# Kernel tuning notes

Measured on AMD Instinct MI355X. Metric: run time of the kernel, lower is better.

Reference implementation:

```python
import jax, jax.numpy as jnp
import numpy as np

GROUPS = 8
NEG_SLOPE = 0.1
EPS = 1e-5


def group_norm(x, gamma, beta):
    # x: (B, N, C). Matches torch GroupNorm applied on (B, C, N):
    # normalize over (channels-in-group, N) per batch per group.
    B, N, C = x.shape
    xg = x.reshape(B, N, GROUPS, C // GROUPS)
    mean = xg.mean(axis=(1, 3), keepdims=True)
    var = xg.var(axis=(1, 3), keepdims=True)
    xg = (xg - mean) * jax.lax.rsqrt(var + EPS)
    return xg.reshape(B, N, C) * gamma + beta


def unary_block(x, W, b, gamma, beta):
    # Linear -> GroupNorm -> LeakyReLU(0.1)
    h = jnp.einsum('bnc,cd->bnd', x, W) + b
    h = group_norm(h, gamma, beta)
    return jnp.where(h >= 0, h, NEG_SLOPE * h)


def setup_inputs() -> dict:
    key = jax.random.key(0)
    ks = jax.random.split(key, 16)
    B, N, M, K, Cin, Cout = 4, 8192, 32768, 16, 128, 128
    inp = {
        'q_feats': jax.random.normal(ks[0], (B, N, Cin), jnp.float32),
        's_feats': jax.random.normal(ks[1], (B, M, Cin), jnp.float32),
        'q_points': jax.random.normal(ks[2], (B, N, 3), jnp.float32),
        's_points': jax.random.normal(ks[3], (B, N, K, 3), jnp.float32),
        'downsample_indices': jax.random.randint(ks[4], (B, N, K), 0, M, jnp.int32),
    }
    sc1 = 1.0 / np.sqrt(Cin)
    sc2 = 1.0 / np.sqrt(Cout)
    inp['W1'] = jax.random.uniform(ks[5], (Cin, Cout), jnp.float32, -sc1, sc1)
    inp['b1'] = jnp.zeros((Cout,), jnp.float32)
    inp['g1'] = jnp.ones((Cout,), jnp.float32)
    inp['be1'] = jnp.zeros((Cout,), jnp.float32)
    inp['W2'] = jax.random.uniform(ks[6], (Cout, Cout), jnp.float32, -sc2, sc2)
    inp['b2'] = jnp.zeros((Cout,), jnp.float32)
    inp['g2'] = jnp.ones((Cout,), jnp.float32)
    inp['be2'] = jnp.zeros((Cout,), jnp.float32)
    inp['W3'] = jax.random.uniform(ks[7], (Cout, Cout), jnp.float32, -sc2, sc2)
    inp['b3'] = jnp.zeros((Cout,), jnp.float32)
    inp['g3'] = jnp.ones((Cout,), jnp.float32)
    inp['be3'] = jnp.zeros((Cout,), jnp.float32)
    return inp


def reference(q_feats, s_feats, q_points, s_points, downsample_indices,
              W1, b1, g1, be1, W2, b2, g2, be2, W3, b3, g3, be3):
    # knn_gather: (B, N, K, C) gathered from (B, M, C)
    grouped = jax.vmap(lambda f, i: f[i])(s_feats, downsample_indices)
    # inverse-squared-distance weights over K neighbors
    d2 = jnp.sum((s_points - q_points[:, :, None, :]) ** 2, axis=-1)  # (B,N,K)
    w = 1.0 / (d2 + 1e-8)
    w = w / jnp.sum(w, axis=-1, keepdims=True)
    latent = jnp.sum(grouped * w[..., None], axis=2)  # (B,N,C)
    h = unary_block(latent, W1, b1, g1, be1)
    h = unary_block(h, W2, b2, g2, be2)
    return unary_block(h + q_feats, W3, b3, g3, be3)
```

## Files before the change

kernel.cpp:

```cpp
#include <hip/hip_runtime.h>


constexpr int NPB = 8192;
constexpr int BN  = 32768;
constexpr int CH  = 128;
constexpr int KNB = 16;
constexpr int MS  = 32768;
constexpr int NG  = 8;
constexpr int CG  = 16;
constexpr int RPB = 64;
constexpr int NBLK = BN / RPB;
constexpr int BPB  = NPB / RPB;
constexpr int XS = 144;
constexpr int WS = 144;

typedef short short8 __attribute__((ext_vector_type(8)));
typedef float floatx4 __attribute__((ext_vector_type(4)));

__device__ __forceinline__ unsigned short f2bs(float f) {
    unsigned int u = __builtin_bit_cast(unsigned int, f);
    unsigned int r = (u + 0x7fffu + ((u >> 16) & 1u)) >> 16;
    return (unsigned short)r;
}
__device__ __forceinline__ float bs2f(unsigned short s) {
    unsigned int u = ((unsigned int)s) << 16;
    return __builtin_bit_cast(float, u);
}

__global__ __launch_bounds__(256) void k_prep(
    const float* __restrict__ W1, const float* __restrict__ W2,
    const float* __restrict__ W3,
    unsigned short* __restrict__ Wt1, unsigned short* __restrict__ Wt2,
    unsigned short* __restrict__ Wt3)
{
    const int bi = blockIdx.x;
    const int w  = bi >> 6;
    const int i  = bi & 63;
    const int el = i * 256 + threadIdx.x;
    const int n  = el >> 7, k = el & 127;
    const float* W = (w == 0) ? W1 : (w == 1) ? W2 : W3;
    unsigned short* Wt = (w == 0) ? Wt1 : (w == 1) ? Wt2 : Wt3;
    Wt[n * 128 + k] = f2bs(W[k * 128 + n]);
}

template <int MODE>
__global__ __launch_bounds__(256) void k_pass(
    const unsigned short* __restrict__ hin,
    const float* __restrict__ part_in,
    const float* __restrict__ gamma,
    const float* __restrict__ beta,
    const float* __restrict__ qf,
    const float* __restrict__ sf,
    const float* __restrict__ qp,
    const float* __restrict__ sp,
    const int*   __restrict__ idx,
    const unsigned short* __restrict__ Wt,
    const float* __restrict__ bias,
    unsigned short* __restrict__ hout,
    float* __restrict__ part_out)
{
    const int bi = blockIdx.x;
    const int t  = threadIdx.x;
    const int b  = bi / BPB;

    __shared__ unsigned short Xl[RPB * XS];
    __shared__ unsigned short Wl[CH * WS];
    __shared__ float red[16][17];
    __shared__ float2 stats_s[NG];
    __shared__ float wv[RPB * KNB];
    __shared__ float winv[RPB];
    __shared__ float pw[4][16];

    #pragma unroll
    for (int i = 0; i < 8; i++) {
        int el = i * 2048 + t * 8;
        short8 w8 = *(const short8*)(Wt + el);
        *(short8*)&Wl[(el >> 7) * WS + (el & 127)] = w8;
    }

    if (MODE == 0) {
        #pragma unroll
        for (int i = 0; i < 4; i++) {
            int p = i * 256 + t;
            int row = p >> 4, k = p & 15;
            size_t rg = (size_t)bi * RPB + row;
            float qx = qp[rg * 3 + 0], qy = qp[rg * 3 + 1], qz = qp[rg * 3 + 2];
            const float* spp = sp + (rg * KNB + k) * 3;
            float dx = spp[0] - qx, dy = spp[1] - qy, dz = spp[2] - qz;
            wv[p] = 1.0f / (dx * dx + dy * dy + dz * dz + 1e-8f);
        }
        __syncthreads();
        if (t < RPB) {
            float s = 0.f;
            #pragma unroll
            for (int k = 0; k < KNB; k++) s += wv[t * KNB + k];
            winv[t] = 1.0f / s;
        }
        __syncthreads();
        const int grp = t >> 5, c4 = (t & 31) * 4;
        for (int rr = 0; rr < 8; rr++) {
            int row = grp * 8 + rr;
            size_t rg = (size_t)bi * RPB + row;
            const int* ip = idx + rg * KNB;
            float ax = 0.f, ay = 0.f, az = 0.f, aw = 0.f;
            #pragma unroll
            for (int k = 0; k < KNB; k++) {
                int j = ip[k];
                const float4 f = *(const float4*)(sf + ((size_t)b * MS + j) * CH + c4);
                float w = wv[row * KNB + k];
                ax += w * f.x; ay += w * f.y; az += w * f.z; aw += w * f.w;
            }
            float wi = winv[row];
            ushort4 pk;
            pk.x = f2bs(ax * wi); pk.y = f2bs(ay * wi);
            pk.z = f2bs(az * wi); pk.w = f2bs(aw * wi);
            *(ushort4*)&Xl[row * XS + c4] = pk;
        }
    } else {
        {
            int j = t & 15, chunk = t >> 4;
            float acc = 0.f;
            #pragma unroll
            for (int i = 0; i < 8; i++)
                acc += part_in[(size_t)(b * BPB + chunk * 8 + i) * 16 + j];
            red[chunk][j] = acc;
        }
        __syncthreads();
        if (t < NG) {
            float s = 0.f, q = 0.f;
            #pragma unroll
            for (int c = 0; c < 16; c++) { s += red[c][t]; q += red[c][t + 8]; }
            const float cnt = (float)(NPB * CG);
            float mean = s / cnt;
            float var  = q / cnt - mean * mean;
            stats_s[t] = make_float2(mean, rsqrtf(var + 1e-5f));
        }
        __syncthreads();
        #pragma unroll
        for (int i = 0; i < 4; i++) {
            int flat = i * 2048 + t * 8;
            int row = flat >> 7, col = flat & 127;
            size_t gidx = (size_t)bi * RPB * CH + flat;
            short8 hv = *(const short8*)(hin + gidx);
            float2 st = stats_s[col >> 4];
            float4 g0 = *(const float4*)(gamma + col);
            float4 g1 = *(const float4*)(gamma + col + 4);
            float4 b0 = *(const float4*)(beta + col);
            float4 b1 = *(const float4*)(beta + col + 4);
            float gg[8] = {g0.x, g0.y, g0.z, g0.w, g1.x, g1.y, g1.z, g1.w};
            float bb[8] = {b0.x, b0.y, b0.z, b0.w, b1.x, b1.y, b1.z, b1.w};
            float re[8];
            if (MODE == 2) {
                float4 r0 = *(const float4*)(qf + gidx);
                float4 r1 = *(const float4*)(qf + gidx + 4);
                re[0]=r0.x; re[1]=r0.y; re[2]=r0.z; re[3]=r0.w;
                re[4]=r1.x; re[5]=r1.y; re[6]=r1.z; re[7]=r1.w;
            }
            unsigned short ov[8];
            #pragma unroll
            for (int e = 0; e < 8; e++) {
                float v = bs2f((unsigned short)hv[e]);
                float y = (v - st.x) * st.y * gg[e] + bb[e];
                y = (y >= 0.f) ? y : 0.1f * y;
                if (MODE == 2) y += re[e];
                ov[e] = f2bs(y);
            }
            *(short8*)&Xl[row * XS + col] = *(short8*)ov;
        }
    }
    __syncthreads();

    const int w  = t >> 6;
    const int l  = t & 63;
    const int lr = l & 15;
    const int qd = l >> 4;
    floatx4 acc[8] = {};
    #pragma unroll
    for (int kt = 0; kt < 4; kt++) {
        short8 a = *(const short8*)&Xl[(w * 16 + lr) * XS + kt * 32 + qd * 8];
        #pragma unroll
        for (int j = 0; j < 8; j++) {
            short8 bf = *(const short8*)&Wl[(j * 16 + lr) * WS + kt * 32 + qd * 8];
            acc[j] = __builtin_amdgcn_mfma_f32_16x16x32_bf16(a, bf, acc[j], 0, 0, 0);
        }
    }

    float vals[8][4];
    #pragma unroll
    for (int j = 0; j < 8; j++) {
        float bj = bias[j * 16 + lr];
        float ss = 0.f, qq = 0.f;
        #pragma unroll
        for (int r = 0; r < 4; r++) {
            float v = acc[j][r] + bj;
            vals[j][r] = v;
            ss += v; qq += v * v;
        }
        #pragma unroll
        for (int off = 32; off; off >>= 1) {
            ss += __shfl_down(ss, off);
            qq += __shfl_down(qq, off);
        }
        if (l == 0) { pw[w][j] = ss; pw[w][8 + j] = qq; }
    }
    #pragma unroll
    for (int j = 0; j < 8; j++)
        #pragma unroll
        for (int r = 0; r < 4; r++)
            Xl[(w * 16 + qd * 4 + r) * XS + j * 16 + lr] = f2bs(vals[j][r]);
    __syncthreads();
    if (t < 16)
        part_out[(size_t)bi * 16 + t] = pw[0][t] + pw[1][t] + pw[2][t] + pw[3][t];
    #pragma unroll
    for (int i = 0; i < 4; i++) {
        int flat = i * 2048 + t * 8;
        int row = flat >> 7, col = flat & 127;
        *(short8*)(hout + (size_t)bi * RPB * CH + flat) =
            *(const short8*)&Xl[row * XS + col];
    }
}

__global__ __launch_bounds__(256) void k_out(
    const unsigned short* __restrict__ hin, const float* __restrict__ part_in,
    const float* __restrict__ gamma, const float* __restrict__ beta,
    float* __restrict__ out)
{
    const int bi = blockIdx.x;
    const int t  = threadIdx.x;
    const int b  = bi / BPB;
    __shared__ float red[16][17];
    __shared__ float2 stats_s[NG];
    {
        int j = t & 15, chunk = t >> 4;
        float acc = 0.f;
        #pragma unroll
        for (int i = 0; i < 8; i++)
            acc += part_in[(size_t)(b * BPB + chunk * 8 + i) * 16 + j];
        red[chunk][j] = acc;
    }
    __syncthreads();
    if (t < NG) {
        float s = 0.f, q = 0.f;
        #pragma unroll
        for (int c = 0; c < 16; c++) { s += red[c][t]; q += red[c][t + 8]; }
        const float cnt = (float)(NPB * CG);
        float mean = s / cnt;
        float var  = q / cnt - mean * mean;
        stats_s[t] = make_float2(mean, rsqrtf(var + 1e-5f));
    }
    __syncthreads();
    #pragma unroll
    for (int i = 0; i < 4; i++) {
        int flat = i * 2048 + t * 8;
        int col = flat & 127;
        size_t gidx = (size_t)bi * RPB * CH + flat;
        short8 hv = *(const short8*)(hin + gidx);
        float2 st = stats_s[col >> 4];
        float4 g0 = *(const float4*)(gamma + col);
        float4 g1 = *(const float4*)(gamma + col + 4);
        float4 b0 = *(const float4*)(beta + col);
        float4 b1 = *(const float4*)(beta + col + 4);
        float gg[8] = {g0.x, g0.y, g0.z, g0.w, g1.x, g1.y, g1.z, g1.w};
        float bb[8] = {b0.x, b0.y, b0.z, b0.w, b1.x, b1.y, b1.z, b1.w};
        float o[8];
        #pragma unroll
        for (int e = 0; e < 8; e++) {
            float v = bs2f((unsigned short)hv[e]);
            float y = (v - st.x) * st.y * gg[e] + bb[e];
            o[e] = (y >= 0.f) ? y : 0.1f * y;
        }
        float4 o0 = {o[0], o[1], o[2], o[3]};
        float4 o1 = {o[4], o[5], o[6], o[7]};
        *(float4*)(out + gidx)     = o0;
        *(float4*)(out + gidx + 4) = o1;
    }
}

extern "C" void kernel_launch(void* const* d_in, const int* in_sizes, int n_in,
                              void* d_out, int out_size, void* d_ws, size_t ws_size,
                              hipStream_t stream) {
    const float* qf  = (const float*)d_in[0];
    const float* sf  = (const float*)d_in[1];
    const float* qp  = (const float*)d_in[2];
    const float* sp  = (const float*)d_in[3];
    const int*   idx = (const int*)  d_in[4];
    const float* W1  = (const float*)d_in[5];
    const float* b1  = (const float*)d_in[6];
    const float* g1  = (const float*)d_in[7];
    const float* be1 = (const float*)d_in[8];
    const float* W2  = (const float*)d_in[9];
    const float* b2  = (const float*)d_in[10];
    const float* g2  = (const float*)d_in[11];
    const float* be2 = (const float*)d_in[12];
    const float* W3  = (const float*)d_in[13];
    const float* b3  = (const float*)d_in[14];
    const float* g3  = (const float*)d_in[15];
    const float* be3 = (const float*)d_in[16];

    char* ws = (char*)d_ws;
    unsigned short* Wt1 = (unsigned short*)(ws);
    unsigned short* Wt2 = (unsigned short*)(ws + 32768);
    unsigned short* Wt3 = (unsigned short*)(ws + 65536);
    float* p1 = (float*)(ws + 98304);
    float* p2 = (float*)(ws + 131072);
    float* p3 = (float*)(ws + 163840);
    unsigned short* h1 = (unsigned short*)(ws + 196608);
    unsigned short* h2 = (unsigned short*)(ws + 196608 + 8388608);
    unsigned short* h3 = (unsigned short*)(ws + 196608 + 2 * 8388608);
    float* out = (float*)d_out;

    k_prep<<<192, 256, 0, stream>>>(W1, W2, W3, Wt1, Wt2, Wt3);
    k_pass<0><<<NBLK, 256, 0, stream>>>(nullptr, nullptr, nullptr, nullptr,
                                        nullptr, sf, qp, sp, idx,
                                        Wt1, b1, h1, p1);
    k_pass<1><<<NBLK, 256, 0, stream>>>(h1, p1, g1, be1, nullptr,
                                        nullptr, nullptr, nullptr, nullptr,
                                        Wt2, b2, h2, p2);
    k_pass<2><<<NBLK, 256, 0, stream>>>(h2, p2, g2, be2, qf,
                                        nullptr, nullptr, nullptr, nullptr,
                                        Wt3, b3, h3, p3);
    k_out<<<NBLK, 256, 0, stream>>>(h3, p3, g3, be3, out);
}
```

Measured before the change: 195.4 us.

## Fuse all three unary blocks into one persistent kernel with grid barriers

Replaces the four per-stage kernels with a single kernel that holds each block's GEMM output in registers across stages. Group-norm statistics are accumulated with global atomics, and an atomic-counter grid barrier separates the stages. This removes the bf16 intermediate writes and reads to global memory and the extra kernel launches, and remaps block indices so each XCD handles one batch. It also pads the LDS row stride. In exchange it depends on all 512 blocks being resident at once to avoid deadlock, and the float atomics make the statistics summation order nondeterministic.

```diff
diff --git a/kernel.cpp b/kernel.cpp
--- a/kernel.cpp
+++ b/kernel.cpp
@@ -11,29 +11,39 @@
 constexpr int RPB = 64;
 constexpr int NBLK = BN / RPB;
 constexpr int BPB  = NPB / RPB;
-constexpr int XS = 144;
-constexpr int WS = 144;
+constexpr int XS = 152;
+constexpr int WS = 152;
 
 typedef short short8 __attribute__((ext_vector_type(8)));
 typedef float floatx4 __attribute__((ext_vector_type(4)));
 
-__device__ __forceinline__ unsigned short f2bs(float f) {
+static __device__ __forceinline__ unsigned short f2bs(float f) {
     unsigned int u = __builtin_bit_cast(unsigned int, f);
     unsigned int r = (u + 0x7fffu + ((u >> 16) & 1u)) >> 16;
     return (unsigned short)r;
 }
-__device__ __forceinline__ float bs2f(unsigned short s) {
-    unsigned int u = ((unsigned int)s) << 16;
-    return __builtin_bit_cast(float, u);
+
+static __device__ __forceinline__ void gbar(unsigned int* bar, unsigned int target) {
+    __syncthreads();
+    if (threadIdx.x == 0) {
+        __hip_atomic_fetch_add(bar, 1u, __ATOMIC_ACQ_REL, __HIP_MEMORY_SCOPE_AGENT);
+        unsigned int v;
+        do {
+            __builtin_amdgcn_s_sleep(2);
+            v = __hip_atomic_load(bar, __ATOMIC_ACQUIRE, __HIP_MEMORY_SCOPE_AGENT);
+        } while (v < target);
+    }
+    __syncthreads();
 }
 
 __global__ __launch_bounds__(256) void k_prep(
     const float* __restrict__ W1, const float* __restrict__ W2,
     const float* __restrict__ W3,
     unsigned short* __restrict__ Wt1, unsigned short* __restrict__ Wt2,
-    unsigned short* __restrict__ Wt3)
+    unsigned short* __restrict__ Wt3, float* __restrict__ accs)
 {
     const int bi = blockIdx.x;
+    if (bi == 0) accs[threadIdx.x] = 0.f;
     const int w  = bi >> 6;
     const int i  = bi & 63;
     const int el = i * 256 + threadIdx.x;
@@ -43,60 +53,129 @@
     Wt[n * 128 + k] = f2bs(W[k * 128 + n]);
 }
 
-template <int MODE>
-__global__ __launch_bounds__(256) void k_pass(
-    const unsigned short* __restrict__ hin,
-    const float* __restrict__ part_in,
-    const float* __restrict__ gamma,
-    const float* __restrict__ beta,
+__global__ __launch_bounds__(256, 2) void k_fused(
+    const float* __restrict__ sf, const float* __restrict__ qp,
+    const float* __restrict__ sp, const int* __restrict__ idx,
     const float* __restrict__ qf,
-    const float* __restrict__ sf,
-    const float* __restrict__ qp,
-    const float* __restrict__ sp,
-    const int*   __restrict__ idx,
-    const unsigned short* __restrict__ Wt,
-    const float* __restrict__ bias,
-    unsigned short* __restrict__ hout,
-    float* __restrict__ part_out)
+    const unsigned short* __restrict__ Wt1,
+    const unsigned short* __restrict__ Wt2,
+    const unsigned short* __restrict__ Wt3,
+    const float* __restrict__ b1, const float* __restrict__ g1, const float* __restrict__ be1,
+    const float* __restrict__ b2, const float* __restrict__ g2, const float* __restrict__ be2,
+    const float* __restrict__ b3, const float* __restrict__ g3, const float* __restrict__ be3,
+    float* __restrict__ accs,
+    unsigned int* __restrict__ bar,
+    float* __restrict__ out)
 {
-    const int bi = blockIdx.x;
-    const int t  = threadIdx.x;
-    const int b  = bi / BPB;
+    const int p   = blockIdx.x;
+    const int xcd = p & 7, q = p >> 3;
+    const int bi  = (xcd >> 1) * BPB + (xcd & 1) * 64 + q;
+    const int b   = xcd >> 1;
+    const int t   = threadIdx.x;
+    const int w   = t >> 6;
+    const int l   = t & 63;
+    const int lr  = l & 15;
+    const int qd  = l >> 4;
 
     __shared__ unsigned short Xl[RPB * XS];
     __shared__ unsigned short Wl[CH * WS];
-    __shared__ float red[16][17];
     __shared__ float2 stats_s[NG];
     __shared__ float wv[RPB * KNB];
     __shared__ float winv[RPB];
     __shared__ float pw[4][16];
 
+    float vals[8][4];
+
+    auto stageW = [&](const unsigned short* __restrict__ Wt) {
+        #pragma unroll
+        for (int i = 0; i < 8; i++) {
+            int el = i * 2048 + t * 8;
+            short8 w8 = *(const short8*)(Wt + el);
+            *(short8*)&Wl[(el >> 7) * WS + (el & 127)] = w8;
+        }
+    };
+
+    auto do_gemm = [&](const float* __restrict__ bias, float* accL) {
+        floatx4 acc[8] = {};
+        #pragma unroll
+        for (int kt = 0; kt < 4; kt++) {
+            short8 a = *(const short8*)&Xl[(w * 16 + lr) * XS + kt * 32 + qd * 8];
+            #pragma unroll
+            for (int j = 0; j < 8; j++) {
+                short8 bf = *(const short8*)&Wl[(j * 16 + lr) * WS + kt * 32 + qd * 8];
+                acc[j] = __builtin_amdgcn_mfma_f32_16x16x32_bf16(a, bf, acc[j], 0, 0, 0);
+            }
+        }
+        #pragma unroll
+        for (int j = 0; j < 8; j++) {
+            float bj = bias[j * 16 + lr];
+            float ss = 0.f, qq = 0.f;
+            #pragma unroll
+            for (int r = 0; r < 4; r++) {
+                float v = acc[j][r] + bj;
+                vals[j][r] = v;
+                ss += v; qq += v * v;
+            }
+            #pragma unroll
+            for (int off = 32; off; off >>= 1) {
+                ss += __shfl_down(ss, off);
+                qq += __shfl_down(qq, off);
+            }
+            if (l == 0) { pw[w][j] = ss; pw[w][8 + j] = qq; }
+        }
+        __syncthreads();
+        if (t < 16)
+            atomicAdd(&accL[b * 16 + t], pw[0][t] + pw[1][t] + pw[2][t] + pw[3][t]);
+    };
+
+    auto gn_apply = [&](float* accL, const float* __restrict__ g,
+                        const float* __restrict__ be, const float* __restrict__ resid) {
+        if (t < 8) {
+            float s  = __hip_atomic_load(accL + b * 16 + t,     __ATOMIC_ACQUIRE, __HIP_MEMORY_SCOPE_AGENT);
+            float q2 = __hip_atomic_load(accL + b * 16 + 8 + t, __ATOMIC_ACQUIRE, __HIP_MEMORY_SCOPE_AGENT);
+            const float cnt = (float)(NPB * CG);
+            float mean = s / cnt;
+            float var  = q2 / cnt - mean * mean;
+            stats_s[t] = make_float2(mean, rsqrtf(var + 1e-5f));
+        }
+        __syncthreads();
+        #pragma unroll
+        for (int j = 0; j < 8; j++) {
+            const int c = j * 16 + lr;
+            float2 st = stats_s[j];
+            float ga = g[c], bb = be[c];
+            #pragma unroll
+            for (int r = 0; r < 4; r++) {
+                float y = (vals[j][r] - st.x) * st.y * ga + bb;
+                y = (y >= 0.f) ? y : 0.1f * y;
+                if (resid)
+                    y += resid[((size_t)bi * RPB + w * 16 + qd * 4 + r) * CH + c];
+                Xl[(w * 16 + qd * 4 + r) * XS + c] = f2bs(y);
+            }
+        }
+        __syncthreads();
+    };
+
+    stageW(Wt1);
     #pragma unroll
-    for (int i = 0; i < 8; i++) {
-        int el = i * 2048 + t * 8;
-        short8 w8 = *(const short8*)(Wt + el);
-        *(short8*)&Wl[(el >> 7) * WS + (el & 127)] = w8;
-    }
-
-    if (MODE == 0) {
-        #pragma unroll
-        for (int i = 0; i < 4; i++) {
-            int p = i * 256 + t;
-            int row = p >> 4, k = p & 15;
-            size_t rg = (size_t)bi * RPB + row;
-            float qx = qp[rg * 3 + 0], qy = qp[rg * 3 + 1], qz = qp[rg * 3 + 2];
-            const float* spp = sp + (rg * KNB + k) * 3;
-            float dx = spp[0] - qx, dy = spp[1] - qy, dz = spp[2] - qz;
-            wv[p] = 1.0f / (dx * dx + dy * dy + dz * dz + 1e-8f);
-        }
-        __syncthreads();
-        if (t < RPB) {
-            float s = 0.f;
-            #pragma unroll
-            for (int k = 0; k < KNB; k++) s += wv[t * KNB + k];
-            winv[t] = 1.0f / s;
-        }
-        __syncthreads();
+    for (int i = 0; i < 4; i++) {
+        int pk = i * 256 + t;
+        int row = pk >> 4, k = pk & 15;
+        size_t rg = (size_t)bi * RPB + row;
+        float qx = qp[rg * 3 + 0], qy = qp[rg * 3 + 1], qz = qp[rg * 3 + 2];
+        const float* spp = sp + (rg * KNB + k) * 3;
+        float dx = spp[0] - qx, dy = spp[1] - qy, dz = spp[2] - qz;
+        wv[pk] = 1.0f / (dx * dx + dy * dy + dz * dz + 1e-8f);
+    }
+    __syncthreads();
+    if (t < RPB) {
+        float s = 0.f;
+        #pragma unroll
+        for (int k = 0; k < KNB; k++) s += wv[t * KNB + k];
+        winv[t] = 1.0f / s;
+    }
+    __syncthreads();
+    {
         const int grp = t >> 5, c4 = (t & 31) * 4;
         for (int rr = 0; rr < 8; rr++) {
             int row = grp * 8 + rr;
@@ -107,172 +186,51 @@
             for (int k = 0; k < KNB; k++) {
                 int j = ip[k];
                 const float4 f = *(const float4*)(sf + ((size_t)b * MS + j) * CH + c4);
-                float w = wv[row * KNB + k];
-                ax += w * f.x; ay += w * f.y; az += w * f.z; aw += w * f.w;
+                float ww = wv[row * KNB + k];
+                ax += ww * f.x; ay += ww * f.y; az += ww * f.z; aw += ww * f.w;
             }
             float wi = winv[row];
-            ushort4 pk;
-            pk.x = f2bs(ax * wi); pk.y = f2bs(ay * wi);
-            pk.z = f2bs(az * wi); pk.w = f2bs(aw * wi);
-            *(ushort4*)&Xl[row * XS + c4] = pk;
-        }
-    } else {
-        {
-            int j = t & 15, chunk = t >> 4;
-            float acc = 0.f;
-            #pragma unroll
-            for (int i = 0; i < 8; i++)
-                acc += part_in[(size_t)(b * BPB + chunk * 8 + i) * 16 + j];
-            red[chunk][j] = acc;
-        }
-        __syncthreads();
-        if (t < NG) {
-            float s = 0.f, q = 0.f;
-            #pragma unroll
-            for (int c = 0; c < 16; c++) { s += red[c][t]; q += red[c][t + 8]; }
-            const float cnt = (float)(NPB * CG);
-            float mean = s / cnt;
-            float var  = q / cnt - mean * mean;
-            stats_s[t] = make_float2(mean, rsqrtf(var + 1e-5f));
-        }
-        __syncthreads();
-        #pragma unroll
-        for (int i = 0; i < 4; i++) {
-            int flat = i * 2048 + t * 8;
-            int row = flat >> 7, col = flat & 127;
-            size_t gidx = (size_t)bi * RPB * CH + flat;
-            short8 hv = *(const short8*)(hin + gidx);
-            float2 st = stats_s[col >> 4];
-            float4 g0 = *(const float4*)(gamma + col);
-            float4 g1 = *(const float4*)(gamma + col + 4);
-            float4 b0 = *(const float4*)(beta + col);
-            float4 b1 = *(const float4*)(beta + col + 4);
-            float gg[8] = {g0.x, g0.y, g0.z, g0.w, g1.x, g1.y, g1.z, g1.w};
-            float bb[8] = {b0.x, b0.y, b0.z, b0.w, b1.x, b1.y, b1.z, b1.w};
-            float re[8];
-            if (MODE == 2) {
-                float4 r0 = *(const float4*)(qf + gidx);
-                float4 r1 = *(const float4*)(qf + gidx + 4);
-                re[0]=r0.x; re[1]=r0.y; re[2]=r0.z; re[3]=r0.w;
-                re[4]=r1.x; re[5]=r1.y; re[6]=r1.z; re[7]=r1.w;
-            }
-            unsigned short ov[8];
-            #pragma unroll
-            for (int e = 0; e < 8; e++) {
-                float v = bs2f((unsigned short)hv[e]);
-                float y = (v - st.x) * st.y * gg[e] + bb[e];
-                y = (y >= 0.f) ? y : 0.1f * y;
-                if (MODE == 2) y += re[e];
-                ov[e] = f2bs(y);
-            }
-            *(short8*)&Xl[row * XS + col] = *(short8*)ov;
-        }
-    }
-    __syncthreads();
-
-    const int w  = t >> 6;
-    const int l  = t & 63;
-    const int lr = l & 15;
-    const int qd = l >> 4;
-    floatx4 acc[8] = {};
-    #pragma unroll
-    for (int kt = 0; kt < 4; kt++) {
-        short8 a = *(const short8*)&Xl[(w * 16 + lr) * XS + kt * 32 + qd * 8];
-        #pragma unroll
-        for (int j = 0; j < 8; j++) {
-            short8 bf = *(const short8*)&Wl[(j * 16 + lr) * WS + kt * 32 + qd * 8];
-            acc[j] = __builtin_amdgcn_mfma_f32_16x16x32_bf16(a, bf, acc[j], 0, 0, 0);
-        }
-    }
-
-    float vals[8][4];
+            ushort4 pkv;
+            pkv.x = f2bs(ax * wi); pkv.y = f2bs(ay * wi);
+            pkv.z = f2bs(az * wi); pkv.w = f2bs(aw * wi);
+            *(ushort4*)&Xl[row * XS + c4] = pkv;
+        }
+    }
+    __syncthreads();
+
+    do_gemm(b1, accs + 0);
+    stageW(Wt2);
+    gbar(bar, 1 * NBLK);
+
+    gn_apply(accs + 0, g1, be1, nullptr);
+    do_gemm(b2, accs + 64);
+    stageW(Wt3);
+    gbar(bar, 2 * NBLK);
+
+    gn_apply(accs + 64, g2, be2, qf);
+    do_gemm(b3, accs + 128);
+    gbar(bar, 3 * NBLK);
+
+    if (t < 8) {
+        float s  = __hip_atomic_load(accs + 128 + b * 16 + t,     __ATOMIC_ACQUIRE, __HIP_MEMORY_SCOPE_AGENT);
+        float q2 = __hip_atomic_load(accs + 128 + b * 16 + 8 + t, __ATOMIC_ACQUIRE, __HIP_MEMORY_SCOPE_AGENT);
+        const float cnt = (float)(NPB * CG);
+        float mean = s / cnt;
+        float var  = q2 / cnt - mean * mean;
+        stats_s[t] = make_float2(mean, rsqrtf(var + 1e-5f));
+    }
+    __syncthreads();
     #pragma unroll
     for (int j = 0; j < 8; j++) {
-        float bj = bias[j * 16 + lr];
-        float ss = 0.f, qq = 0.f;
+        const int c = j * 16 + lr;
+        float2 st = stats_s[j];
+        float ga = g3[c], bb = be3[c];
         #pragma unroll
         for (int r = 0; r < 4; r++) {
-            float v = acc[j][r] + bj;
-            vals[j][r] = v;
-            ss += v; qq += v * v;
-        }
-        #pragma unroll
-        for (int off = 32; off; off >>= 1) {
-            ss += __shfl_down(ss, off);
-            qq += __shfl_down(qq, off);
-        }
-        if (l == 0) { pw[w][j] = ss; pw[w][8 + j] = qq; }
-    }
-    #pragma unroll
-    for (int j = 0; j < 8; j++)
-        #pragma unroll
-        for (int r = 0; r < 4; r++)
-            Xl[(w * 16 + qd * 4 + r) * XS + j * 16 + lr] = f2bs(vals[j][r]);
-    __syncthreads();
-    if (t < 16)
-        part_out[(size_t)bi * 16 + t] = pw[0][t] + pw[1][t] + pw[2][t] + pw[3][t];
-    #pragma unroll
-    for (int i = 0; i < 4; i++) {
-        int flat = i * 2048 + t * 8;
-        int row = flat >> 7, col = flat & 127;
-        *(short8*)(hout + (size_t)bi * RPB * CH + flat) =
-            *(const short8*)&Xl[row * XS + col];
-    }
-}
-
-__global__ __launch_bounds__(256) void k_out(
-    const unsigned short* __restrict__ hin, const float* __restrict__ part_in,
-    const float* __restrict__ gamma, const float* __restrict__ beta,
-    float* __restrict__ out)
-{
-    const int bi = blockIdx.x;
-    const int t  = threadIdx.x;
-    const int b  = bi / BPB;
-    __shared__ float red[16][17];
-    __shared__ float2 stats_s[NG];
-    {
-        int j = t & 15, chunk = t >> 4;
-        float acc = 0.f;
-        #pragma unroll
-        for (int i = 0; i < 8; i++)
-            acc += part_in[(size_t)(b * BPB + chunk * 8 + i) * 16 + j];
-        red[chunk][j] = acc;
-    }
-    __syncthreads();
-    if (t < NG) {
-        float s = 0.f, q = 0.f;
-        #pragma unroll
-        for (int c = 0; c < 16; c++) { s += red[c][t]; q += red[c][t + 8]; }
-        const float cnt = (float)(NPB * CG);
-        float mean = s / cnt;
-        float var  = q / cnt - mean * mean;
-        stats_s[t] = make_float2(mean, rsqrtf(var + 1e-5f));
-    }
-    __syncthreads();
-    #pragma unroll
-    for (int i = 0; i < 4; i++) {
-        int flat = i * 2048 + t * 8;
-        int col = flat & 127;
-        size_t gidx = (size_t)bi * RPB * CH + flat;
-        short8 hv = *(const short8*)(hin + gidx);
-        float2 st = stats_s[col >> 4];
-        float4 g0 = *(const float4*)(gamma + col);
-        float4 g1 = *(const float4*)(gamma + col + 4);
-        float4 b0 = *(const float4*)(beta + col);
-        float4 b1 = *(const float4*)(beta + col + 4);
-        float gg[8] = {g0.x, g0.y, g0.z, g0.w, g1.x, g1.y, g1.z, g1.w};
-        float bb[8] = {b0.x, b0.y, b0.z, b0.w, b1.x, b1.y, b1.z, b1.w};
-        float o[8];
-        #pragma unroll
-        for (int e = 0; e < 8; e++) {
-            float v = bs2f((unsigned short)hv[e]);
-            float y = (v - st.x) * st.y * gg[e] + bb[e];
-            o[e] = (y >= 0.f) ? y : 0.1f * y;
-        }
-        float4 o0 = {o[0], o[1], o[2], o[3]};
-        float4 o1 = {o[4], o[5], o[6], o[7]};
-        *(float4*)(out + gidx)     = o0;
-        *(float4*)(out + gidx + 4) = o1;
+            float y = (vals[j][r] - st.x) * st.y * ga + bb;
+            y = (y >= 0.f) ? y : 0.1f * y;
+            out[((size_t)bi * RPB + w * 16 + qd * 4 + r) * CH + c] = y;
+        }
     }
 }
 
@@ -301,23 +259,15 @@
     unsigned short* Wt1 = (unsigned short*)(ws);
     unsigned short* Wt2 = (unsigned short*)(ws + 32768);
     unsigned short* Wt3 = (unsigned short*)(ws + 65536);
-    float* p1 = (float*)(ws + 98304);
-    float* p2 = (float*)(ws + 131072);
-    float* p3 = (float*)(ws + 163840);
-    unsigned short* h1 = (unsigned short*)(ws + 196608);
-    unsigned short* h2 = (unsigned short*)(ws + 196608 + 8388608);
-    unsigned short* h3 = (unsigned short*)(ws + 196608 + 2 * 8388608);
+    float* accs = (float*)(ws + 98304);
+    unsigned int* bar = (unsigned int*)(ws + 98304 + 192 * 4);
     float* out = (float*)d_out;
 
-    k_prep<<<192, 256, 0, stream>>>(W1, W2, W3, Wt1, Wt2, Wt3);
-    k_pass<0><<<NBLK, 256, 0, stream>>>(nullptr, nullptr, nullptr, nullptr,
-                                        nullptr, sf, qp, sp, idx,
-                                        Wt1, b1, h1, p1);
-    k_pass<1><<<NBLK, 256, 0, stream>>>(h1, p1, g1, be1, nullptr,
-                                        nullptr, nullptr, nullptr, nullptr,
-                                        Wt2, b2, h2, p2);
-    k_pass<2><<<NBLK, 256, 0, stream>>>(h2, p2, g2, be2, qf,
-                                        nullptr, nullptr, nullptr, nullptr,
-                                        Wt3, b3, h3, p3);
-    k_out<<<NBLK, 256, 0, stream>>>(h3, p3, g3, be3, out);
-}
+    k_prep<<<192, 256, 0, stream>>>(W1, W2, W3, Wt1, Wt2, Wt3, accs);
+    k_fused<<<NBLK, 256, 0, stream>>>(sf, qp, sp, idx, qf,
+                                      Wt1, Wt2, Wt3,
+                                      b1, g1, be1,
+                                      b2, g2, be2,
+                                      b3, g3, be3,
+                                      accs, bar, out);
+}
```

After: 356.0 us. 82.1% more time.

## Pre-swizzle W2/W3 into MFMA fragment order and read B directly from global

Applied to the files above, without the earlier changes.

Splits the templated pass kernel into a gather head kernel and a middle kernel. The prep kernel writes W2 and W3 in MFMA-fragment order, so the middle kernels load B operands straight from global or L2 instead of staging the 32KB weight matrix in LDS. This removes the LDS weight copy and cuts LDS footprint, which may allow more resident blocks. LDS row stride is also changed from 144 to 152 to alter the bank mapping. The cost is more repeated global or L2 reads of the weights per block.

```diff
diff --git a/kernel.cpp b/kernel.cpp
--- a/kernel.cpp
+++ b/kernel.cpp
@@ -11,18 +11,18 @@
 constexpr int RPB = 64;
 constexpr int NBLK = BN / RPB;
 constexpr int BPB  = NPB / RPB;
-constexpr int XS = 144;
-constexpr int WS = 144;
+constexpr int XS = 152;
+constexpr int WS = 152;
 
 typedef short short8 __attribute__((ext_vector_type(8)));
 typedef float floatx4 __attribute__((ext_vector_type(4)));
 
-__device__ __forceinline__ unsigned short f2bs(float f) {
+static __device__ __forceinline__ unsigned short f2bs(float f) {
     unsigned int u = __builtin_bit_cast(unsigned int, f);
     unsigned int r = (u + 0x7fffu + ((u >> 16) & 1u)) >> 16;
     return (unsigned short)r;
 }
-__device__ __forceinline__ float bs2f(unsigned short s) {
+static __device__ __forceinline__ float bs2f(unsigned short s) {
     unsigned int u = ((unsigned int)s) << 16;
     return __builtin_bit_cast(float, u);
 }
@@ -30,8 +30,8 @@
 __global__ __launch_bounds__(256) void k_prep(
     const float* __restrict__ W1, const float* __restrict__ W2,
     const float* __restrict__ W3,
-    unsigned short* __restrict__ Wt1, unsigned short* __restrict__ Wt2,
-    unsigned short* __restrict__ Wt3)
+    unsigned short* __restrict__ Wt1, unsigned short* __restrict__ Wf2,
+    unsigned short* __restrict__ Wf3)
 {
     const int bi = blockIdx.x;
     const int w  = bi >> 6;
@@ -39,21 +39,20 @@
     const int el = i * 256 + threadIdx.x;
     const int n  = el >> 7, k = el & 127;
     const float* W = (w == 0) ? W1 : (w == 1) ? W2 : W3;
-    unsigned short* Wt = (w == 0) ? Wt1 : (w == 1) ? Wt2 : Wt3;
-    Wt[n * 128 + k] = f2bs(W[k * 128 + n]);
-}
-
-template <int MODE>
-__global__ __launch_bounds__(256) void k_pass(
-    const unsigned short* __restrict__ hin,
-    const float* __restrict__ part_in,
-    const float* __restrict__ gamma,
-    const float* __restrict__ beta,
-    const float* __restrict__ qf,
-    const float* __restrict__ sf,
-    const float* __restrict__ qp,
-    const float* __restrict__ sp,
-    const int*   __restrict__ idx,
+    unsigned short v = f2bs(W[k * 128 + n]);
+    if (w == 0) {
+        Wt1[n * 128 + k] = v;
+    } else {
+        unsigned short* Wf = (w == 1) ? Wf2 : Wf3;
+        int j = n >> 4, lr = n & 15;
+        int kt = k >> 5, qd = (k >> 3) & 3, e = k & 7;
+        Wf[(((j * 4 + kt) * 64) + (qd * 16 + lr)) * 8 + e] = v;
+    }
+}
+
+__global__ __launch_bounds__(256) void k_head(
+    const float* __restrict__ sf, const float* __restrict__ qp,
+    const float* __restrict__ sp, const int* __restrict__ idx,
     const unsigned short* __restrict__ Wt,
     const float* __restrict__ bias,
     unsigned short* __restrict__ hout,
@@ -65,8 +64,6 @@
 
     __shared__ unsigned short Xl[RPB * XS];
     __shared__ unsigned short Wl[CH * WS];
-    __shared__ float red[16][17];
-    __shared__ float2 stats_s[NG];
     __shared__ float wv[RPB * KNB];
     __shared__ float winv[RPB];
     __shared__ float pw[4][16];
@@ -78,25 +75,25 @@
         *(short8*)&Wl[(el >> 7) * WS + (el & 127)] = w8;
     }
 
-    if (MODE == 0) {
-        #pragma unroll
-        for (int i = 0; i < 4; i++) {
-            int p = i * 256 + t;
-            int row = p >> 4, k = p & 15;
-            size_t rg = (size_t)bi * RPB + row;
-            float qx = qp[rg * 3 + 0], qy = qp[rg * 3 + 1], qz = qp[rg * 3 + 2];
-            const float* spp = sp + (rg * KNB + k) * 3;
-            float dx = spp[0] - qx, dy = spp[1] - qy, dz = spp[2] - qz;
-            wv[p] = 1.0f / (dx * dx + dy * dy + dz * dz + 1e-8f);
-        }
-        __syncthreads();
-        if (t < RPB) {
-            float s = 0.f;
-            #pragma unroll
-            for (int k = 0; k < KNB; k++) s += wv[t * KNB + k];
-            winv[t] = 1.0f / s;
-        }
-        __syncthreads();
+    #pragma unroll
+    for (int i = 0; i < 4; i++) {
+        int p = i * 256 + t;
+        int row = p >> 4, k = p & 15;
+        size_t rg = (size_t)bi * RPB + row;
+        float qx = qp[rg * 3 + 0], qy = qp[rg * 3 + 1], qz = qp[rg * 3 + 2];
+        const float* spp = sp + (rg * KNB + k) * 3;
+        float dx = spp[0] - qx, dy = spp[1] - qy, dz = spp[2] - qz;
+        wv[p] = 1.0f / (dx * dx + dy * dy + dz * dz + 1e-8f);
+    }
+    __syncthreads();
+    if (t < RPB) {
+        float s = 0.f;
+        #pragma unroll
+        for (int k = 0; k < KNB; k++) s += wv[t * KNB + k];
+        winv[t] = 1.0f / s;
+    }
+    __syncthreads();
+    {
         const int grp = t >> 5, c4 = (t & 31) * 4;
         for (int rr = 0; rr < 8; rr++) {
             int row = grp * 8 + rr;
@@ -116,57 +113,6 @@
             pk.z = f2bs(az * wi); pk.w = f2bs(aw * wi);
             *(ushort4*)&Xl[row * XS + c4] = pk;
         }
-    } else {
-        {
-            int j = t & 15, chunk = t >> 4;
-            float acc = 0.f;
-            #pragma unroll
-            for (int i = 0; i < 8; i++)
-                acc += part_in[(size_t)(b * BPB + chunk * 8 + i) * 16 + j];
-            red[chunk][j] = acc;
-        }
-        __syncthreads();
-        if (t < NG) {
-            float s = 0.f, q = 0.f;
-            #pragma unroll
-            for (int c = 0; c < 16; c++) { s += red[c][t]; q += red[c][t + 8]; }
-            const float cnt = (float)(NPB * CG);
-            float mean = s / cnt;
-            float var  = q / cnt - mean * mean;
-            stats_s[t] = make_float2(mean, rsqrtf(var + 1e-5f));
-        }
-        __syncthreads();
-        #pragma unroll
-        for (int i = 0; i < 4; i++) {
-            int flat = i * 2048 + t * 8;
-            int row = flat >> 7, col = flat & 127;
-            size_t gidx = (size_t)bi * RPB * CH + flat;
-            short8 hv = *(const short8*)(hin + gidx);
-            float2 st = stats_s[col >> 4];
-            float4 g0 = *(const float4*)(gamma + col);
-            float4 g1 = *(const float4*)(gamma + col + 4);
-            float4 b0 = *(const float4*)(beta + col);
-            float4 b1 = *(const float4*)(beta + col + 4);
-            float gg[8] = {g0.x, g0.y, g0.z, g0.w, g1.x, g1.y, g1.z, g1.w};
-            float bb[8] = {b0.x, b0.y, b0.z, b0.w, b1.x, b1.y, b1.z, b1.w};
-            float re[8];
-            if (MODE == 2) {
-                float4 r0 = *(const float4*)(qf + gidx);
-                float4 r1 = *(const float4*)(qf + gidx + 4);
-                re[0]=r0.x; re[1]=r0.y; re[2]=r0.z; re[3]=r0.w;
-                re[4]=r1.x; re[5]=r1.y; re[6]=r1.z; re[7]=r1.w;
-            }
-            unsigned short ov[8];
-            #pragma unroll
-            for (int e = 0; e < 8; e++) {
-                float v = bs2f((unsigned short)hv[e]);
-                float y = (v - st.x) * st.y * gg[e] + bb[e];
-                y = (y >= 0.f) ? y : 0.1f * y;
-                if (MODE == 2) y += re[e];
-                ov[e] = f2bs(y);
-            }
-            *(short8*)&Xl[row * XS + col] = *(short8*)ov;
-        }
     }
     __syncthreads();
 
@@ -181,6 +127,129 @@
         #pragma unroll
         for (int j = 0; j < 8; j++) {
             short8 bf = *(const short8*)&Wl[(j * 16 + lr) * WS + kt * 32 + qd * 8];
+            acc[j] = __builtin_amdgcn_mfma_f32_16x16x32_bf16(a, bf, acc[j], 0, 0, 0);
+        }
+    }
+
+    float vals[8][4];
+    #pragma unroll
+    for (int j = 0; j < 8; j++) {
+        float bj = bias[j * 16 + lr];
+        float ss = 0.f, qq = 0.f;
+        #pragma unroll
+        for (int r = 0; r < 4; r++) {
+            float v = acc[j][r] + bj;
+            vals[j][r] = v;
+            ss += v; qq += v * v;
+        }
+        #pragma unroll
+        for (int off = 32; off; off >>= 1) {
+            ss += __shfl_down(ss, off);
+            qq += __shfl_down(qq, off);
+        }
+        if (l == 0) { pw[w][j] = ss; pw[w][8 + j] = qq; }
+    }
+    #pragma unroll
+    for (int j = 0; j < 8; j++)
+        #pragma unroll
+        for (int r = 0; r < 4; r++)
+            Xl[(w * 16 + qd * 4 + r) * XS + j * 16 + lr] = f2bs(vals[j][r]);
+    __syncthreads();
+    if (t < 16)
+        part_out[(size_t)bi * 16 + t] = pw[0][t] + pw[1][t] + pw[2][t] + pw[3][t];
+    #pragma unroll
+    for (int i = 0; i < 4; i++) {
+        int flat = i * 2048 + t * 8;
+        int row = flat >> 7, col = flat & 127;
+        *(short8*)(hout + (size_t)bi * RPB * CH + flat) =
+            *(const short8*)&Xl[row * XS + col];
+    }
+}
+
+template <int RESID>
+__global__ __launch_bounds__(256) void k_mid(
+    const unsigned short* __restrict__ hin,
+    const float* __restrict__ part_in,
+    const float* __restrict__ gamma,
+    const float* __restrict__ beta,
+    const float* __restrict__ qf,
+    const unsigned short* __restrict__ Wf,
+    const float* __restrict__ bias,
+    unsigned short* __restrict__ hout,
+    float* __restrict__ part_out)
+{
+    const int bi = blockIdx.x;
+    const int t  = threadIdx.x;
+    const int b  = bi / BPB;
+
+    __shared__ unsigned short Xl[RPB * XS];
+    __shared__ float red[16][17];
+    __shared__ float2 stats_s[NG];
+    __shared__ float pw[4][16];
+
+    {
+        int j = t & 15, chunk = t >> 4;
+        float acc = 0.f;
+        #pragma unroll
+        for (int i = 0; i < 8; i++)
+            acc += part_in[(size_t)(b * BPB + chunk * 8 + i) * 16 + j];
+        red[chunk][j] = acc;
+    }
+    __syncthreads();
+    if (t < NG) {
+        float s = 0.f, q = 0.f;
+        #pragma unroll
+        for (int c = 0; c < 16; c++) { s += red[c][t]; q += red[c][t + 8]; }
+        const float cnt = (float)(NPB * CG);
+        float mean = s / cnt;
+        float var  = q / cnt - mean * mean;
+        stats_s[t] = make_float2(mean, rsqrtf(var + 1e-5f));
+    }
+    __syncthreads();
+    #pragma unroll
+    for (int i = 0; i < 4; i++) {
+        int flat = i * 2048 + t * 8;
+        int row = flat >> 7, col = flat & 127;
+        size_t gidx = (size_t)bi * RPB * CH + flat;
+        short8 hv = *(const short8*)(hin + gidx);
+        float2 st = stats_s[col >> 4];
+        float4 g0 = *(const float4*)(gamma + col);
+        float4 g1 = *(const float4*)(gamma + col + 4);
+        float4 b0 = *(const float4*)(beta + col);
+        float4 b1 = *(const float4*)(beta + col + 4);
+        float gg[8] = {g0.x, g0.y, g0.z, g0.w, g1.x, g1.y, g1.z, g1.w};
+        float bb[8] = {b0.x, b0.y, b0.z, b0.w, b1.x, b1.y, b1.z, b1.w};
+        float re[8];
+        if (RESID) {
+            float4 r0 = *(const float4*)(qf + gidx);
+            float4 r1 = *(const float4*)(qf + gidx + 4);
+            re[0]=r0.x; re[1]=r0.y; re[2]=r0.z; re[3]=r0.w;
+            re[4]=r1.x; re[5]=r1.y; re[6]=r1.z; re[7]=r1.w;
+        }
+        unsigned short ov[8];
+        #pragma unroll
+        for (int e = 0; e < 8; e++) {
+            float v = bs2f((unsigned short)hv[e]);
+            float y = (v - st.x) * st.y * gg[e] + bb[e];
+            y = (y >= 0.f) ? y : 0.1f * y;
+            if (RESID) y += re[e];
+            ov[e] = f2bs(y);
+        }
+        *(short8*)&Xl[row * XS + col] = *(short8*)ov;
+    }
+    __syncthreads();
+
+    const int w  = t >> 6;
+    const int l  = t & 63;
+    const int lr = l & 15;
+    const int qd = l >> 4;
+    floatx4 acc[8] = {};
+    #pragma unroll
+    for (int kt = 0; kt < 4; kt++) {
+        short8 a = *(const short8*)&Xl[(w * 16 + lr) * XS + kt * 32 + qd * 8];
+        #pragma unroll
+        for (int j = 0; j < 8; j++) {
+            short8 bf = *(const short8*)(Wf + (((j * 4 + kt) * 64) + l) * 8);
             acc[j] = __builtin_amdgcn_mfma_f32_16x16x32_bf16(a, bf, acc[j], 0, 0, 0);
         }
     }
@@ -299,8 +368,8 @@
 
     char* ws = (char*)d_ws;
     unsigned short* Wt1 = (unsigned short*)(ws);
-    unsigned short* Wt2 = (unsigned short*)(ws + 32768);
-    unsigned short* Wt3 = (unsigned short*)(ws + 65536);
+    unsigned short* Wf2 = (unsigned short*)(ws + 32768);
+    unsigned short* Wf3 = (unsigned short*)(ws + 65536);
     float* p1 = (float*)(ws + 98304);
     float* p2 = (float*)(ws + 131072);
     float* p3 = (float*)(ws + 163840);
@@ -309,15 +378,9 @@
     unsigned short* h3 = (unsigned short*)(ws + 196608 + 2 * 8388608);
     float* out = (float*)d_out;
 
-    k_prep<<<192, 256, 0, stream>>>(W1, W2, W3, Wt1, Wt2, Wt3);
-    k_pass<0><<<NBLK, 256, 0, stream>>>(nullptr, nullptr, nullptr, nullptr,
-                                        nullptr, sf, qp, sp, idx,
-                                        Wt1, b1, h1, p1);
-    k_pass<1><<<NBLK, 256, 0, stream>>>(h1, p1, g1, be1, nullptr,
-                                        nullptr, nullptr, nullptr, nullptr,
-                                        Wt2, b2, h2, p2);
-    k_pass<2><<<NBLK, 256, 0, stream>>>(h2, p2, g2, be2, qf,
-                                        nullptr, nullptr, nullptr, nullptr,
-                                        Wt3, b3, h3, p3);
+    k_prep<<<192, 256, 0, stream>>>(W1, W2, W3, Wt1, Wf2, Wf3);
+    k_head<<<NBLK, 256, 0, stream>>>(sf, qp, sp, idx, Wt1, b1, h1, p1);
+    k_mid<0><<<NBLK, 256, 0, stream>>>(h1, p1, g1, be1, nullptr, Wf2, b2, h2, p2);
+    k_mid<1><<<NBLK, 256, 0, stream>>>(h2, p2, g2, be2, qf, Wf3, b3, h3, p3);
     k_out<<<NBLK, 256, 0, stream>>>(h3, p3, g3, be3, out);
 }
```

New measurement: 198.1 us. About the same (+1.4%).
